# Kernel optimization log

Hardware: AMD Instinct MI355X
Metric: run time of the kernel (lower is better)

## Reference

```python
import jax, jax.numpy as jnp
import numpy as np

EPS = 1e-5

def layernorm(x, w, b):
    mu = jnp.mean(x, axis=-1, keepdims=True)
    xc = x - mu
    var = jnp.mean(xc * xc, axis=-1, keepdims=True)
    return xc * jax.lax.rsqrt(var + EPS) * w + b

def setup_inputs() -> dict:
    key = jax.random.key(0)
    ks = jax.random.split(key, 9)
    B, T, Nm, Nl = 8, 8, 1024, 64
    Vw, Tw, H, Dh = 1024, 2048, 8, 64
    inner = H * Dh  # 512
    s_q = 1.0 / np.sqrt(Tw)
    s_kv = 1.0 / np.sqrt(Vw)
    s_o = 1.0 / np.sqrt(inner)
    return {
        "x": jax.random.normal(ks[0], (B, T, Nm, Vw), jnp.float32),
        "latents": jax.random.normal(ks[1], (B, T, Nl, Tw), jnp.float32),
        "nm_w": jnp.ones((Vw,), jnp.float32),
        "nm_b": jnp.zeros((Vw,), jnp.float32),
        "nl_w": jnp.ones((Tw,), jnp.float32),
        "nl_b": jnp.zeros((Tw,), jnp.float32),
        "Wq": jax.random.normal(ks[2], (Tw, inner), jnp.float32) * s_q,
        "Wkv": jax.random.normal(ks[3], (Vw, 2 * inner), jnp.float32) * s_kv,
        "Wout": jax.random.normal(ks[4], (inner, Tw), jnp.float32) * s_o,
    }

def reference(x, latents, nm_w, nm_b, nl_w, nl_b, Wq, Wkv, Wout):
    H, Dh = 8, 64
    scale = Dh ** (-0.5)
    B, T, Nm, _ = x.shape
    Nl = latents.shape[2]
    xn = layernorm(x, nm_w, nm_b)          # (B,T,Nm,Vw)
    ln = layernorm(latents, nl_w, nl_b)    # (B,T,Nl,Tw)
    q = (ln @ Wq).reshape(B, T, Nl, H, Dh)           # b t i h d
    kv = xn @ Wkv                                     # (B,T,Nm,2*inner)
    k, v = jnp.split(kv, 2, axis=-1)
    k = k.reshape(B, T, Nm, H, Dh)                    # b t j h d
    v = v.reshape(B, T, Nm, H, Dh)
    sim = jnp.einsum('btihd,btjhd->bthij', q * scale, k)  # (B,T,H,Nl,Nm)
    attn = jax.nn.softmax(sim, axis=-1)
    out = jnp.einsum('bthij,btjhd->btihd', attn, v)       # (B,T,Nl,H,Dh)
    out = out.reshape(B, T, Nl, H * Dh)
    return out @ Wout                                     # (B,T,Nl,Tw)
```

## Files before the change

kernel.cpp:

```cpp
#include <hip/hip_runtime.h>

typedef __attribute__((ext_vector_type(8))) short bfrag8;
typedef __attribute__((ext_vector_type(4))) float f32x4;

typedef const unsigned int __attribute__((address_space(1)))* gas1_u32;
typedef unsigned int __attribute__((address_space(3)))* gas3_u32;

#define DEV __device__ __forceinline__

DEV unsigned short f2bf(float f) {
  unsigned int u = __builtin_bit_cast(unsigned int, f);
  u += 0x7fffu + ((u >> 16) & 1u);
  return (unsigned short)(u >> 16);
}

DEV void gload_lds16(const void* g, void* l) {
  __builtin_amdgcn_global_load_lds((gas1_u32)g, (gas3_u32)l, 16, 0, 0);
}

__global__ __launch_bounds__(256) void k_pre(
    const float* __restrict__ x, unsigned short* __restrict__ xb,
    float* __restrict__ mu, float* __restrict__ rstd,
    const float* __restrict__ lat, const float* __restrict__ nl_w,
    const float* __restrict__ nl_b, unsigned short* __restrict__ lnb,
    const float* __restrict__ Wq,   unsigned short* __restrict__ WqT,
    const float* __restrict__ Wkv,  unsigned short* __restrict__ WkvT,
    const float* __restrict__ Wout, unsigned short* __restrict__ WoutT,
    const float* __restrict__ nm_w, const float* __restrict__ nm_b,
    float* __restrict__ part)
{
  __shared__ float smem[32 * 33];
  const int bid = blockIdx.x, tid = threadIdx.x;
  const int wid = tid >> 6, lane = tid & 63;

  if (bid < 16384) {
    const int row = bid * 4 + wid;
    const float* base = x + (size_t)row * 1024;
    float4 v[4];
    #pragma unroll
    for (int i = 0; i < 4; ++i) v[i] = ((const float4*)base)[i * 64 + lane];
    float s = 0.f, q = 0.f;
    #pragma unroll
    for (int i = 0; i < 4; ++i) {
      s += v[i].x + v[i].y + v[i].z + v[i].w;
      q += v[i].x*v[i].x + v[i].y*v[i].y + v[i].z*v[i].z + v[i].w*v[i].w;
    }
    #pragma unroll
    for (int off = 32; off >= 1; off >>= 1) { s += __shfl_xor(s, off); q += __shfl_xor(q, off); }
    const float m  = s * (1.0f/1024.0f);
    const float var = q * (1.0f/1024.0f) - m * m;
    const float rs = rsqrtf(var + 1e-5f);
    if (lane == 0) { mu[row] = m; rstd[row] = rs; }
    unsigned short* ob = xb + (size_t)row * 1024;
    #pragma unroll
    for (int i = 0; i < 4; ++i) {
      ushort4 o;
      o.x = f2bf(v[i].x); o.y = f2bf(v[i].y); o.z = f2bf(v[i].z); o.w = f2bf(v[i].w);
      ((ushort4*)ob)[i * 64 + lane] = o;
    }
    return;
  }
  if (bid < 20480) {
    const int row = bid - 16384;
    const float* base = lat + (size_t)row * 2048;
    const float4 v0 = ((const float4*)base)[tid];
    const float4 v1 = ((const float4*)base)[256 + tid];
    float s = v0.x+v0.y+v0.z+v0.w + v1.x+v1.y+v1.z+v1.w;
    float q = v0.x*v0.x+v0.y*v0.y+v0.z*v0.z+v0.w*v0.w
            + v1.x*v1.x+v1.y*v1.y+v1.z*v1.z+v1.w*v1.w;
    #pragma unroll
    for (int off = 32; off >= 1; off >>= 1) { s += __shfl_xor(s, off); q += __shfl_xor(q, off); }
    if (lane == 0) { smem[wid] = s; smem[4 + wid] = q; }
    __syncthreads();
    s = smem[0] + smem[1] + smem[2] + smem[3];
    q = smem[4] + smem[5] + smem[6] + smem[7];
    const float m  = s * (1.0f/2048.0f);
    const float var = q * (1.0f/2048.0f) - m * m;
    const float rs = rsqrtf(var + 1e-5f);
    const float4 w0 = ((const float4*)nl_w)[tid], w1 = ((const float4*)nl_w)[256 + tid];
    const float4 b0 = ((const float4*)nl_b)[tid], b1 = ((const float4*)nl_b)[256 + tid];
    ushort4 o0, o1;
    o0.x = f2bf((v0.x - m) * rs * w0.x + b0.x);
    o0.y = f2bf((v0.y - m) * rs * w0.y + b0.y);
    o0.z = f2bf((v0.z - m) * rs * w0.z + b0.z);
    o0.w = f2bf((v0.w - m) * rs * w0.w + b0.w);
    o1.x = f2bf((v1.x - m) * rs * w1.x + b1.x);
    o1.y = f2bf((v1.y - m) * rs * w1.y + b1.y);
    o1.z = f2bf((v1.z - m) * rs * w1.z + b1.z);
    o1.w = f2bf((v1.w - m) * rs * w1.w + b1.w);
    ((ushort4*)(lnb + (size_t)row * 2048))[tid] = o0;
    ((ushort4*)(lnb + (size_t)row * 2048))[256 + tid] = o1;
    return;
  }
  if (bid < 23552) {
    int tb = bid - 20480;
    const float* src; unsigned short* dst; int Kd, N; const float* rsc; float sc;
    if (tb < 1024)      { src = Wq;   dst = WqT;   Kd = 2048; N = 512;  rsc = nullptr; sc = 0.125f; }
    else if (tb < 2048) { tb -= 1024; src = Wkv;  dst = WkvT;  Kd = 1024; N = 1024; rsc = nm_w;   sc = 1.0f; }
    else                { tb -= 2048; src = Wout; dst = WoutT; Kd = 512;  N = 2048; rsc = nullptr; sc = 1.0f; }
    float (*tile)[33] = (float(*)[33])smem;
    const int tx = tid & 31, ty = tid >> 5;
    const int ntiles = N >> 5;
    const int k0 = (tb / ntiles) << 5;
    const int n0 = (tb % ntiles) << 5;
    #pragma unroll
    for (int r = 0; r < 4; ++r) {
      const int kk = ty + r * 8;
      float v = src[(size_t)(k0 + kk) * N + n0 + tx] * sc;
      if (rsc) v *= rsc[k0 + kk];
      tile[kk][tx] = v;
    }
    __syncthreads();
    #pragma unroll
    for (int r = 0; r < 4; ++r) {
      const int nn = ty + r * 8;
      dst[(size_t)(n0 + nn) * Kd + k0 + tx] = f2bf(tile[tx][nn]);
    }
    return;
  }
  {
    const int cb = bid - 23552;
    const int kc = cb >> 2;
    const int n  = (cb & 3) * 256 + tid;
    float s1 = 0.f, s2 = 0.f;
    const int k0 = kc * 64;
    for (int k = k0; k < k0 + 64; ++k) {
      const float wv = Wkv[(size_t)k * 1024 + n];
      s1 += nm_w[k] * wv;
      s2 += nm_b[k] * wv;
    }
    part[(size_t)(kc * 2 + 0) * 1024 + n] = s1;
    part[(size_t)(kc * 2 + 1) * 1024 + n] = s2;
  }
}

__global__ __launch_bounds__(256) void k_c1c2_red(
    const float* __restrict__ part, float* __restrict__ c1, float* __restrict__ c2)
{
  const int n = blockIdx.x * 256 + threadIdx.x;
  float s1 = 0.f, s2 = 0.f;
  #pragma unroll
  for (int kc = 0; kc < 16; ++kc) {
    s1 += part[(size_t)(kc * 2 + 0) * 1024 + n];
    s2 += part[(size_t)(kc * 2 + 1) * 1024 + n];
  }
  c1[n] = s1; c2[n] = s2;
}

#define BAR8   __builtin_amdgcn_s_barrier()
#define GATE4  asm volatile("s_waitcnt vmcnt(4)\n\ts_barrier" ::: "memory")

__global__ __launch_bounds__(512, 2) void k_mm(
    const unsigned short* __restrict__ A,
    const unsigned short* __restrict__ Bt,
    unsigned short* __restrict__ C,
    const float* __restrict__ mu, const float* __restrict__ rstd,
    const float* __restrict__ c1, const float* __restrict__ c2,
    const unsigned short* __restrict__ Aq,
    const unsigned short* __restrict__ Bq,
    unsigned short* __restrict__ Cq)
{
  __shared__ __attribute__((aligned(16))) char lds[131072];
  const int tid = threadIdx.x;
  const int wid = tid >> 6, lane = tid & 63;
  const int g = lane >> 4, c = lane & 15;

  if (blockIdx.x < 1024) {
    constexpr int NKT = 16;
    int bid = blockIdx.x;
    bid = (bid & 7) * 128 + (bid >> 3);
    const int mt = bid >> 2, nt = bid & 3;
    const int wr = wid >> 2, wc = wid & 3;
    const int MO = wr * 128, NO = wc * 64;

    const unsigned short* gA = A + (size_t)mt * 256 * 1024;
    const unsigned short* gB = Bt + (size_t)nt * 256 * 1024;

    const f32x4 zz = {0.f, 0.f, 0.f, 0.f};
    f32x4 acc[8][4];
    #pragma unroll
    for (int m = 0; m < 8; ++m)
      #pragma unroll
      for (int n = 0; n < 4; ++n) acc[m][n] = zz;

    auto stageA = [&](int buf, int kk, int kt) {
      #pragma unroll
      for (int i = 0; i < 2; ++i) {
        const int o = (i * 512 + tid) * 16;
        const int row = o >> 6;
        const int ss = ((((o >> 4) & 3) - (row >> 1)) & 3);
        gload_lds16((const char*)(gA + (size_t)row * 1024 + kt * 64 + kk * 32) + ss * 16,
                    lds + buf * 32768 + kk * 16384 + o);
      }
    };
    auto stageB = [&](int buf, int kk, int kt) {
      #pragma unroll
      for (int i = 0; i < 2; ++i) {
        const int o = (i * 512 + tid) * 16;
        const int row = o >> 6;
        const int ss = ((((o >> 4) & 3) - (row >> 1)) & 3);
        gload_lds16((const char*)(gB + (size_t)row * 1024 + kt * 64 + kk * 32) + ss * 16,
                    lds + 65536 + buf * 32768 + kk * 16384 + o);
      }
    };
    auto rdA = [&](int buf, int kk, int m) -> bfrag8 {
      const int row = MO + m * 16 + c;
      return *(const bfrag8*)(lds + buf * 32768 + kk * 16384 + row * 64
                              + (((g + (row >> 1)) & 3) << 4));
    };
    auto rdB = [&](int buf, int kk, int n) -> bfrag8 {
      const int row = NO + n * 16 + c;
      return *(const bfrag8*)(lds + 65536 + buf * 32768 + kk * 16384 + row * 64
                              + (((g + (row >> 1)) & 3) << 4));
    };

    bfrag8 a[8], b0[4], b1[4];

    auto tile4 = [&](int buf, int sb, int ukt) {
      #pragma unroll
      for (int m = 0; m < 8; ++m) a[m] = rdA(buf, 0, m);
      #pragma unroll
      for (int n = 0; n < 4; ++n) b0[n] = rdB(buf, 0, n);
      stageA(sb, 0, ukt);
      __builtin_amdgcn_s_setprio(1);
      #pragma unroll
      for (int m = 0; m < 8; ++m) {
        acc[m][0] = __builtin_amdgcn_mfma_f32_16x16x32_bf16(a[m], b0[0], acc[m][0], 0, 0, 0);
        acc[m][1] = __builtin_amdgcn_mfma_f32_16x16x32_bf16(a[m], b0[1], acc[m][1], 0, 0, 0);
      }
      __builtin_amdgcn_s_setprio(0);
      GATE4;
      #pragma unroll
      for (int n = 0; n < 4; ++n) b1[n] = rdB(buf, 1, n);
      stageB(sb, 0, ukt);
      __builtin_amdgcn_s_setprio(1);
      #pragma unroll
      for (int m = 0; m < 8; ++m) {
        acc[m][2] = __builtin_amdgcn_mfma_f32_16x16x32_bf16(a[m], b0[2], acc[m][2], 0, 0, 0);
        acc[m][3] = __builtin_amdgcn_mfma_f32_16x16x32_bf16(a[m], b0[3], acc[m][3], 0, 0, 0);
      }
      __builtin_amdgcn_s_setprio(0);
      GATE4;
      #pragma unroll
      for (int m = 0; m < 8; ++m) a[m] = rdA(buf, 1, m);
      stageB(sb, 1, ukt);
      __builtin_amdgcn_s_setprio(1);
      #pragma unroll
      for (int m = 0; m < 8; ++m) {
        acc[m][0] = __builtin_amdgcn_mfma_f32_16x16x32_bf16(a[m], b1[0], acc[m][0], 0, 0, 0);
        acc[m][1] = __builtin_amdgcn_mfma_f32_16x16x32_bf16(a[m], b1[1], acc[m][1], 0, 0, 0);
      }
      __builtin_amdgcn_s_setprio(0);
      BAR8;
      stageA(sb, 1, ukt);
      __builtin_amdgcn_s_setprio(1);
      #pragma unroll
      for (int m = 0; m < 8; ++m) {
        acc[m][2] = __builtin_amdgcn_mfma_f32_16x16x32_bf16(a[m], b1[2], acc[m][2], 0, 0, 0);
        acc[m][3] = __builtin_amdgcn_mfma_f32_16x16x32_bf16(a[m], b1[3], acc[m][3], 0, 0, 0);
      }
      __builtin_amdgcn_s_setprio(0);
      GATE4;
    };

    stageA(0, 0, 0); stageB(0, 0, 0); stageB(0, 1, 0); stageA(0, 1, 0);
    GATE4;

    for (int t = 0; t < NKT; t += 2) {
      const int u2 = (t + 2 < NKT) ? t + 2 : 0;
      tile4(0, 1, t + 1);
      tile4(1, 0, u2);
    }
    asm volatile("s_waitcnt vmcnt(0)" ::: "memory");

    #pragma unroll
    for (int m = 0; m < 8; ++m) {
      #pragma unroll
      for (int j = 0; j < 4; ++j) {
        const size_t orow = (size_t)mt * 256 + MO + m * 16 + g * 4 + j;
        const float rs = rstd[orow], muv = mu[orow];
        #pragma unroll
        for (int n = 0; n < 4; ++n) {
          const int gcol = nt * 256 + NO + n * 16 + c;
          const float v = rs * (acc[m][n][j] - muv * c1[gcol]) + c2[gcol];
          C[orow * 1024 + gcol] = f2bf(v);
        }
      }
    }
    return;
  }

  {
    constexpr int BK = 64, MF = 4, NF = 2;
    int lb = blockIdx.x - 1024;
    lb = (lb & 7) * 16 + (lb >> 3);
    const int mt = lb >> 1, nt = lb & 1;
    const int NO = (wid & 7) * 32;
    const int MO = 0;

    const unsigned short* gA = Aq + (size_t)mt * 64 * 2048;
    const unsigned short* gB = Bq + (size_t)nt * 256 * 2048;
    auto asb = [&](int buf) { return lds + buf * 8192; };
    auto bsb = [&](int buf) { return lds + 16384 + buf * 32768; };

    const f32x4 zz = {0.f, 0.f, 0.f, 0.f};
    f32x4 acc[MF][NF];
    #pragma unroll
    for (int m = 0; m < MF; ++m)
      #pragma unroll
      for (int n = 0; n < NF; ++n) acc[m][n] = zz;

    auto stage = [&](int buf, int kt) {
      {
        const int o = tid * 16;
        const int row = o >> 7;
        const int sg = (((o >> 4) & 7) - row) & 7;
        gload_lds16((const char*)(gA + (size_t)row * 2048 + kt * BK) + sg * 16,
                    asb(buf) + o);
      }
      #pragma unroll
      for (int i = 0; i < 4; ++i) {
        const int o = (i * 512 + tid) * 16;
        const int row = o >> 7;
        const int sg = (((o >> 4) & 7) - row) & 7;
        gload_lds16((const char*)(gB + (size_t)row * 2048 + kt * BK) + sg * 16,
                    bsb(buf) + o);
      }
    };
    auto compute = [&](int buf) {
      #pragma unroll
      for (int kk = 0; kk < 2; ++kk) {
        bfrag8 af[MF], bf[NF];
        #pragma unroll
        for (int m = 0; m < MF; ++m) {
          const int rw = MO + m * 16 + c;
          af[m] = *(const bfrag8*)((const char*)asb(buf) + rw * 128
                                   + (((kk * 4 + g + rw) & 7) << 4));
        }
        #pragma unroll
        for (int n = 0; n < NF; ++n) {
          const int rw = NO + n * 16 + c;
          bf[n] = *(const bfrag8*)((const char*)bsb(buf) + rw * 128
                                   + (((kk * 4 + g + rw) & 7) << 4));
        }
        #pragma unroll
        for (int m = 0; m < MF; ++m)
          #pragma unroll
          for (int n = 0; n < NF; ++n)
            acc[m][n] = __builtin_amdgcn_mfma_f32_16x16x32_bf16(af[m], bf[n], acc[m][n], 0, 0, 0);
      }
    };

    const int nkt = 2048 / BK;
    stage(0, 0);
    __syncthreads();
    for (int t = 0; t < nkt; t += 2) {
      if (t + 1 < nkt) stage(1, t + 1);
      compute(0);
      __syncthreads();
      if (t + 2 < nkt) stage(0, t + 2);
      if (t + 1 < nkt) compute(1);
      __syncthreads();
    }

    #pragma unroll
    for (int m = 0; m < MF; ++m) {
      #pragma unroll
      for (int j = 0; j < 4; ++j) {
        const size_t orow = (size_t)mt * 64 + MO + m * 16 + g * 4 + j;
        #pragma unroll
        for (int n = 0; n < NF; ++n) {
          const int gcol = nt * 256 + NO + n * 16 + c;
          Cq[orow * 512 + gcol] = f2bf(acc[m][n][j]);
        }
      }
    }
  }
}

template<int BM, int BN, int WM, int WN, int NT, int MODE>
__global__ __launch_bounds__(NT, 2) void k_gemm(
    const unsigned short* __restrict__ A, int lda,
    const unsigned short* __restrict__ Bt, int ldb,
    int K, int mtiles, int ntiles,
    void* __restrict__ Cout, int ldc)
{
  constexpr int BK = 64;
  constexpr int NW = NT / 64;
  constexpr int MF = (BM / WM) / 16;
  constexpr int NF = (BN / WN) / 16;
  constexpr int LA = (BM * BK) / (8 * NT);
  constexpr int LB = (BN * BK) / (8 * NT);
  static_assert(WM * WN == NW, "wave grid");
  static_assert(LA >= 1 && LB >= 1, "tile too small for NT");

  __shared__ __attribute__((aligned(16))) unsigned short As[2][BM * BK];
  __shared__ __attribute__((aligned(16))) unsigned short Bs[2][BN * BK];

  int bid = blockIdx.x;
  {
    const int nwg = gridDim.x;
    if ((nwg & 7) == 0) {
      const int q = nwg >> 3;
      bid = (bid & 7) * q + (bid >> 3);
    }
  }
  const int mt = bid / ntiles, nt = bid % ntiles;
  const int tid = threadIdx.x;
  const int wid = tid >> 6, lane = tid & 63;
  const int g = lane >> 4, c = lane & 15;
  const int wr = wid / WN, wc = wid % WN;
  const int MO = wr * (BM / WM), NO = wc * (BN / WN);

  const unsigned short* gA = A + (size_t)mt * BM * lda;
  const unsigned short* gB = Bt + (size_t)nt * BN * ldb;

  const f32x4 zz = {0.f, 0.f, 0.f, 0.f};
  f32x4 acc[MF][NF];
  #pragma unroll
  for (int m = 0; m < MF; ++m)
    #pragma unroll
    for (int n = 0; n < NF; ++n) acc[m][n] = zz;

  auto stage = [&](int buf, int kt) {
    #pragma unroll
    for (int i = 0; i < LA; ++i) {
      const int o = (i * NT + tid) * 16;
      const int row = o >> 7;
      const int sg = (((o >> 4) & 7) - row) & 7;
      gload_lds16((const char*)(gA + (size_t)row * lda + kt * BK) + sg * 16,
                  (char*)&As[buf][0] + o);
    }
    #pragma unroll
    for (int i = 0; i < LB; ++i) {
      const int o = (i * NT + tid) * 16;
      const int row = o >> 7;
      const int sg = (((o >> 4) & 7) - row) & 7;
      gload_lds16((const char*)(gB + (size_t)row * ldb + kt * BK) + sg * 16,
                  (char*)&Bs[buf][0] + o);
    }
  };

  auto compute = [&](int buf) {
    #pragma unroll
    for (int kk = 0; kk < 2; ++kk) {
      bfrag8 af[MF], bf[NF];
      #pragma unroll
      for (int m = 0; m < MF; ++m) {
        const int rw = MO + m * 16 + c;
        af[m] = *(const bfrag8*)((const char*)&As[buf][0] + rw * 128
                                 + (((kk * 4 + g + rw) & 7) << 4));
      }
      #pragma unroll
      for (int n = 0; n < NF; ++n) {
        const int rw = NO + n * 16 + c;
        bf[n] = *(const bfrag8*)((const char*)&Bs[buf][0] + rw * 128
                                 + (((kk * 4 + g + rw) & 7) << 4));
      }
      #pragma unroll
      for (int m = 0; m < MF; ++m)
        #pragma unroll
        for (int n = 0; n < NF; ++n)
          acc[m][n] = __builtin_amdgcn_mfma_f32_16x16x32_bf16(af[m], bf[n], acc[m][n], 0, 0, 0);
    }
  };

  const int nkt = K / BK;
  stage(0, 0);
  __syncthreads();
  for (int t = 0; t < nkt; t += 2) {
    if (t + 1 < nkt) stage(1, t + 1);
    compute(0);
    __syncthreads();
    if (t + 2 < nkt) stage(0, t + 2);
    if (t + 1 < nkt) compute(1);
    __syncthreads();
  }

  #pragma unroll
  for (int m = 0; m < MF; ++m) {
    #pragma unroll
    for (int j = 0; j < 4; ++j) {
      const size_t orow = (size_t)mt * BM + MO + m * 16 + g * 4 + j;
      #pragma unroll
      for (int n = 0; n < NF; ++n) {
        const int gcol = nt * BN + NO + n * 16 + c;
        const float v = acc[m][n][j];
        if constexpr (MODE == 2) ((float*)Cout)[orow * ldc + gcol] = v;
        else ((unsigned short*)Cout)[orow * ldc + gcol] = f2bf(v);
      }
    }
  }
}

__global__ __launch_bounds__(256) void k_attn(
    const unsigned short* __restrict__ q,
    const unsigned short* __restrict__ kv,
    unsigned short* __restrict__ ao)
{
  __shared__ __attribute__((aligned(16))) unsigned short Vt[64 * 64];
  const int bid = blockIdx.x;
  const int bt = bid >> 3, h = bid & 7;
  const int tid = threadIdx.x;
  const int wid = tid >> 6, lane = tid & 63;
  const int g = lane >> 4, c = lane & 15;

  const size_t qoff = ((size_t)bt * 64 + wid * 16 + c) * 512 + h * 64;
  const bfrag8 qf0 = *(const bfrag8*)(q + qoff + g * 8);
  const bfrag8 qf1 = *(const bfrag8*)(q + qoff + 32 + g * 8);

  const f32x4 zz = {0.f, 0.f, 0.f, 0.f};
  f32x4 o[4] = {zz, zz, zz, zz};
  float m_run = -1e30f, l_run = 0.f;

  const size_t kvbase = (size_t)bt * 1024 * 1024;
  const unsigned short* kbase = kv + kvbase + h * 64;
  const unsigned short* vbase = kv + kvbase + 512 + h * 64;

  for (int ch = 0; ch < 16; ++ch) {
    #pragma unroll
    for (int rr = 0; rr < 2; ++rr) {
      const int key = rr * 32 + (tid >> 3);
      const int d0 = (tid & 7) * 8;
      const bfrag8 vv = *(const bfrag8*)(vbase + (size_t)(ch * 64 + key) * 1024 + d0);
      #pragma unroll
      for (int j = 0; j < 8; ++j)
        Vt[(d0 + j) * 64 + (key ^ (j << 3))] = (unsigned short)vv[j];
    }
    __syncthreads();
    #pragma unroll
    for (int ks = 0; ks < 2; ++ks) {
      const int kb = ch * 64 + ks * 32;
      f32x4 s[2];
      #pragma unroll
      for (int t = 0; t < 2; ++t) {
        const int kr = ((c >> 2) << 3) + (t << 2) + (c & 3);
        const unsigned short* krow = kbase + (size_t)(kb + kr) * 1024;
        s[t] = zz;
        s[t] = __builtin_amdgcn_mfma_f32_16x16x32_bf16(*(const bfrag8*)(krow + g * 8),      qf0, s[t], 0, 0, 0);
        s[t] = __builtin_amdgcn_mfma_f32_16x16x32_bf16(*(const bfrag8*)(krow + 32 + g * 8), qf1, s[t], 0, 0, 0);
      }
      float pm = s[0][0];
      #pragma unroll
      for (int i = 1; i < 4; ++i) pm = fmaxf(pm, s[0][i]);
      #pragma unroll
      for (int i = 0; i < 4; ++i) pm = fmaxf(pm, s[1][i]);
      pm = fmaxf(pm, __shfl_xor(pm, 16));
      pm = fmaxf(pm, __shfl_xor(pm, 32));
      const float mn = fmaxf(m_run, pm);
      const float alpha = __expf(m_run - mn);
      float p[8];
      #pragma unroll
      for (int i = 0; i < 4; ++i) p[i]     = __expf(s[0][i] - mn);
      #pragma unroll
      for (int i = 0; i < 4; ++i) p[4 + i] = __expf(s[1][i] - mn);
      float ts = 0.f;
      #pragma unroll
      for (int i = 0; i < 8; ++i) ts += p[i];
      ts += __shfl_xor(ts, 16);
      ts += __shfl_xor(ts, 32);
      l_run = l_run * alpha + ts;
      m_run = mn;
      float ar[4];
      #pragma unroll
      for (int rj = 0; rj < 4; ++rj) ar[rj] = __shfl(alpha, g * 4 + rj);
      #pragma unroll
      for (int db = 0; db < 4; ++db)
        #pragma unroll
        for (int j = 0; j < 4; ++j) o[db][j] *= ar[j];
      bfrag8 pa;
      #pragma unroll
      for (int i = 0; i < 8; ++i) pa[i] = (short)f2bf(p[i]);
      #pragma unroll
      for (int db = 0; db < 4; ++db) {
        const int d = db * 16 + c;
        const bfrag8 vb = *(const bfrag8*)(Vt + d * 64 + ((ks * 32 + g * 8) ^ ((c & 7) << 3)));
        o[db] = __builtin_amdgcn_mfma_f32_16x16x32_bf16(pa, vb, o[db], 0, 0, 0);
      }
    }
    __syncthreads();
  }
  float lr[4];
  #pragma unroll
  for (int rj = 0; rj < 4; ++rj) lr[rj] = __shfl(l_run, g * 4 + rj);
  #pragma unroll
  for (int db = 0; db < 4; ++db)
    #pragma unroll
    for (int j = 0; j < 4; ++j) {
      const float val = o[db][j] / lr[j];
      ao[((size_t)bt * 64 + wid * 16 + g * 4 + j) * 512 + h * 64 + db * 16 + c] = f2bf(val);
    }
}

extern "C" void kernel_launch(void* const* d_in, const int* in_sizes, int n_in,
                              void* d_out, int out_size, void* d_ws, size_t ws_size,
                              hipStream_t stream)
{
  const float* x    = (const float*)d_in[0];
  const float* lat  = (const float*)d_in[1];
  const float* nm_w = (const float*)d_in[2];
  const float* nm_b = (const float*)d_in[3];
  const float* nl_w = (const float*)d_in[4];
  const float* nl_b = (const float*)d_in[5];
  const float* Wq   = (const float*)d_in[6];
  const float* Wkv  = (const float*)d_in[7];
  const float* Wout = (const float*)d_in[8];

  char* p = (char*)d_ws;
  auto take = [&](size_t bytes) { char* r = p; p += (bytes + 255) & ~(size_t)255; return r; };
  unsigned short* xb    = (unsigned short*)take(64ull * 1024 * 1024 * 2);
  unsigned short* kvb   = (unsigned short*)take(64ull * 1024 * 1024 * 2);
  unsigned short* lnb   = (unsigned short*)take(4096ull * 2048 * 2);
  unsigned short* qbuf  = (unsigned short*)take(4096ull * 512 * 2);
  unsigned short* aob   = (unsigned short*)take(4096ull * 512 * 2);
  unsigned short* WqT   = (unsigned short*)take(512ull * 2048 * 2);
  unsigned short* WkvT  = (unsigned short*)take(1024ull * 1024 * 2);
  unsigned short* WoutT = (unsigned short*)take(2048ull * 512 * 2);
  float* muv  = (float*)take(65536ull * 4);
  float* rsd  = (float*)take(65536ull * 4);
  float* c1   = (float*)take(1024 * 4);
  float* c2   = (float*)take(1024 * 4);
  float* part = (float*)take(32ull * 1024 * 4);
  if ((size_t)(p - (char*)d_ws) > ws_size) return;

  k_pre<<<dim3(23616), 256, 0, stream>>>(x, xb, muv, rsd,
                                         lat, nl_w, nl_b, lnb,
                                         Wq, WqT, Wkv, WkvT, Wout, WoutT,
                                         nm_w, nm_b, part);
  k_c1c2_red<<<dim3(4), 256, 0, stream>>>(part, c1, c2);

  k_mm<<<dim3(1152), 512, 0, stream>>>(xb, WkvT, kvb, muv, rsd, c1, c2,
                                       lnb, WqT, qbuf);

  k_attn<<<dim3(512), 256, 0, stream>>>(qbuf, kvb, aob);

  k_gemm<64, 128, 1, 4, 256, 2><<<dim3(1024), 256, 0, stream>>>(
      aob, 512, WoutT, 512, 512, 64, 16, d_out, 2048);
}
```

Measured before the change: 356.0 us.

## Fuse x layernorm stats and bf16 conversion into KV GEMM A-loading

Removes the separate pass that read x, computed row mean/rstd and wrote a bf16 copy. The KV GEMM now loads fp32 x directly into registers, converts to bf16 while writing LDS, and accumulates row statistics on the fly for the epilogue. This saves a full 256MB read plus 128MB write round trip. In exchange, each of the four N-tiles re-reads fp32 x (twice the bytes of the bf16 copy), register pressure rises, occupancy drops to one block per CU, and the pipeline schedule changes.

```diff
diff --git a/kernel.cpp b/kernel.cpp
--- a/kernel.cpp
+++ b/kernel.cpp
@@ -19,8 +19,6 @@
 }
 
 __global__ __launch_bounds__(256) void k_pre(
-    const float* __restrict__ x, unsigned short* __restrict__ xb,
-    float* __restrict__ mu, float* __restrict__ rstd,
     const float* __restrict__ lat, const float* __restrict__ nl_w,
     const float* __restrict__ nl_b, unsigned short* __restrict__ lnb,
     const float* __restrict__ Wq,   unsigned short* __restrict__ WqT,
@@ -33,35 +31,8 @@
   const int bid = blockIdx.x, tid = threadIdx.x;
   const int wid = tid >> 6, lane = tid & 63;
 
-  if (bid < 16384) {
-    const int row = bid * 4 + wid;
-    const float* base = x + (size_t)row * 1024;
-    float4 v[4];
-    #pragma unroll
-    for (int i = 0; i < 4; ++i) v[i] = ((const float4*)base)[i * 64 + lane];
-    float s = 0.f, q = 0.f;
-    #pragma unroll
-    for (int i = 0; i < 4; ++i) {
-      s += v[i].x + v[i].y + v[i].z + v[i].w;
-      q += v[i].x*v[i].x + v[i].y*v[i].y + v[i].z*v[i].z + v[i].w*v[i].w;
-    }
-    #pragma unroll
-    for (int off = 32; off >= 1; off >>= 1) { s += __shfl_xor(s, off); q += __shfl_xor(q, off); }
-    const float m  = s * (1.0f/1024.0f);
-    const float var = q * (1.0f/1024.0f) - m * m;
-    const float rs = rsqrtf(var + 1e-5f);
-    if (lane == 0) { mu[row] = m; rstd[row] = rs; }
-    unsigned short* ob = xb + (size_t)row * 1024;
-    #pragma unroll
-    for (int i = 0; i < 4; ++i) {
-      ushort4 o;
-      o.x = f2bf(v[i].x); o.y = f2bf(v[i].y); o.z = f2bf(v[i].z); o.w = f2bf(v[i].w);
-      ((ushort4*)ob)[i * 64 + lane] = o;
-    }
-    return;
-  }
-  if (bid < 20480) {
-    const int row = bid - 16384;
+  if (bid < 4096) {
+    const int row = bid;
     const float* base = lat + (size_t)row * 2048;
     const float4 v0 = ((const float4*)base)[tid];
     const float4 v1 = ((const float4*)base)[256 + tid];
@@ -92,8 +63,8 @@
     ((ushort4*)(lnb + (size_t)row * 2048))[256 + tid] = o1;
     return;
   }
-  if (bid < 23552) {
-    int tb = bid - 20480;
+  if (bid < 7168) {
+    int tb = bid - 4096;
     const float* src; unsigned short* dst; int Kd, N; const float* rsc; float sc;
     if (tb < 1024)      { src = Wq;   dst = WqT;   Kd = 2048; N = 512;  rsc = nullptr; sc = 0.125f; }
     else if (tb < 2048) { tb -= 1024; src = Wkv;  dst = WkvT;  Kd = 1024; N = 1024; rsc = nm_w;   sc = 1.0f; }
@@ -119,7 +90,7 @@
     return;
   }
   {
-    const int cb = bid - 23552;
+    const int cb = bid - 7168;
     const int kc = cb >> 2;
     const int n  = (cb & 3) * 256 + tid;
     float s1 = 0.f, s2 = 0.f;
@@ -147,20 +118,17 @@
   c1[n] = s1; c2[n] = s2;
 }
 
-#define BAR8   __builtin_amdgcn_s_barrier()
-#define GATE4  asm volatile("s_waitcnt vmcnt(4)\n\ts_barrier" ::: "memory")
-
-__global__ __launch_bounds__(512, 2) void k_mm(
-    const unsigned short* __restrict__ A,
+__global__ __launch_bounds__(512, 1) void k_mm(
+    const float* __restrict__ X,
     const unsigned short* __restrict__ Bt,
     unsigned short* __restrict__ C,
-    const float* __restrict__ mu, const float* __restrict__ rstd,
     const float* __restrict__ c1, const float* __restrict__ c2,
     const unsigned short* __restrict__ Aq,
     const unsigned short* __restrict__ Bq,
     unsigned short* __restrict__ Cq)
 {
   __shared__ __attribute__((aligned(16))) char lds[131072];
+  __shared__ float sstat[256][2];
   const int tid = threadIdx.x;
   const int wid = tid >> 6, lane = tid & 63;
   const int g = lane >> 4, c = lane & 15;
@@ -173,8 +141,12 @@
     const int wr = wid >> 2, wc = wid & 3;
     const int MO = wr * 128, NO = wc * 64;
 
-    const unsigned short* gA = A + (size_t)mt * 256 * 1024;
     const unsigned short* gB = Bt + (size_t)nt * 256 * 1024;
+    const int arow = tid >> 1, asl = tid & 1;
+    const int rho = (arow >> 1) & 3;
+    const int ps0 = (2 * asl + 0 + rho) & 3;
+    const int ps1 = (2 * asl + 1 + rho) & 3;
+    const float* gX = X + (size_t)(mt * 256 + arow) * 1024 + asl * 16;
 
     const f32x4 zz = {0.f, 0.f, 0.f, 0.f};
     f32x4 acc[8][4];
@@ -183,15 +155,31 @@
       #pragma unroll
       for (int n = 0; n < 4; ++n) acc[m][n] = zz;
 
-    auto stageA = [&](int buf, int kk, int kt) {
-      #pragma unroll
-      for (int i = 0; i < 2; ++i) {
-        const int o = (i * 512 + tid) * 16;
-        const int row = o >> 6;
-        const int ss = ((((o >> 4) & 3) - (row >> 1)) & 3);
-        gload_lds16((const char*)(gA + (size_t)row * 1024 + kt * 64 + kk * 32) + ss * 16,
-                    lds + buf * 32768 + kk * 16384 + o);
-      }
+    float4 ax[2][4];
+    float ssum = 0.f, sq = 0.f;
+
+    auto loadA = [&](int kt) {
+      #pragma unroll
+      for (int kk = 0; kk < 2; ++kk)
+        #pragma unroll
+        for (int i = 0; i < 4; ++i)
+          ax[kk][i] = *(const float4*)(gX + (size_t)kt * 64 + kk * 32 + i * 4);
+    };
+    auto putA = [&](int buf, int kk, int accum) {
+      unsigned int w[8];
+      #pragma unroll
+      for (int i = 0; i < 4; ++i) {
+        const float4 v = ax[kk][i];
+        if (accum) {
+          ssum += v.x + v.y + v.z + v.w;
+          sq   += v.x*v.x + v.y*v.y + v.z*v.z + v.w*v.w;
+        }
+        w[2*i]   = (unsigned)f2bf(v.x) | ((unsigned)f2bf(v.y) << 16);
+        w[2*i+1] = (unsigned)f2bf(v.z) | ((unsigned)f2bf(v.w) << 16);
+      }
+      char* base = lds + buf * 32768 + kk * 16384 + arow * 64;
+      *(uint4*)(base + ps0 * 16) = make_uint4(w[0], w[1], w[2], w[3]);
+      *(uint4*)(base + ps1 * 16) = make_uint4(w[4], w[5], w[6], w[7]);
     };
     auto stageB = [&](int buf, int kk, int kt) {
       #pragma unroll
@@ -216,12 +204,13 @@
 
     bfrag8 a[8], b0[4], b1[4];
 
-    auto tile4 = [&](int buf, int sb, int ukt) {
+    auto tile4 = [&](int buf, int sb, int ukt, int accum) {
       #pragma unroll
       for (int m = 0; m < 8; ++m) a[m] = rdA(buf, 0, m);
       #pragma unroll
       for (int n = 0; n < 4; ++n) b0[n] = rdB(buf, 0, n);
-      stageA(sb, 0, ukt);
+      loadA(ukt);
+      stageB(sb, 0, ukt);
       __builtin_amdgcn_s_setprio(1);
       #pragma unroll
       for (int m = 0; m < 8; ++m) {
@@ -229,10 +218,11 @@
         acc[m][1] = __builtin_amdgcn_mfma_f32_16x16x32_bf16(a[m], b0[1], acc[m][1], 0, 0, 0);
       }
       __builtin_amdgcn_s_setprio(0);
-      GATE4;
+      asm volatile("s_waitcnt vmcnt(10)\n\ts_barrier" ::: "memory");
       #pragma unroll
       for (int n = 0; n < 4; ++n) b1[n] = rdB(buf, 1, n);
-      stageB(sb, 0, ukt);
+      putA(sb, 0, accum);
+      stageB(sb, 1, ukt);
       __builtin_amdgcn_s_setprio(1);
       #pragma unroll
       for (int m = 0; m < 8; ++m) {
@@ -240,10 +230,10 @@
         acc[m][3] = __builtin_amdgcn_mfma_f32_16x16x32_bf16(a[m], b0[3], acc[m][3], 0, 0, 0);
       }
       __builtin_amdgcn_s_setprio(0);
-      GATE4;
+      asm volatile("s_barrier" ::: "memory");
       #pragma unroll
       for (int m = 0; m < 8; ++m) a[m] = rdA(buf, 1, m);
-      stageB(sb, 1, ukt);
+      putA(sb, 1, accum);
       __builtin_amdgcn_s_setprio(1);
       #pragma unroll
       for (int m = 0; m < 8; ++m) {
@@ -251,8 +241,7 @@
         acc[m][1] = __builtin_amdgcn_mfma_f32_16x16x32_bf16(a[m], b1[1], acc[m][1], 0, 0, 0);
       }
       __builtin_amdgcn_s_setprio(0);
-      BAR8;
-      stageA(sb, 1, ukt);
+      asm volatile("s_barrier" ::: "memory");
       __builtin_amdgcn_s_setprio(1);
       #pragma unroll
       for (int m = 0; m < 8; ++m) {
@@ -260,25 +249,37 @@
         acc[m][3] = __builtin_amdgcn_mfma_f32_16x16x32_bf16(a[m], b1[3], acc[m][3], 0, 0, 0);
       }
       __builtin_amdgcn_s_setprio(0);
-      GATE4;
-    };
-
-    stageA(0, 0, 0); stageB(0, 0, 0); stageB(0, 1, 0); stageA(0, 1, 0);
-    GATE4;
-
-    for (int t = 0; t < NKT; t += 2) {
-      const int u2 = (t + 2 < NKT) ? t + 2 : 0;
-      tile4(0, 1, t + 1);
-      tile4(1, 0, u2);
-    }
-    asm volatile("s_waitcnt vmcnt(0)" ::: "memory");
+      asm volatile("s_waitcnt vmcnt(2) lgkmcnt(0)\n\ts_barrier" ::: "memory");
+    };
+
+    loadA(0);
+    putA(0, 0, 1); putA(0, 1, 1);
+    stageB(0, 0, 0); stageB(0, 1, 0);
+    asm volatile("s_waitcnt vmcnt(0) lgkmcnt(0)\n\ts_barrier" ::: "memory");
+
+    for (int t = 0; t < NKT; ++t) {
+      const int real = (t + 1 < NKT);
+      tile4(t & 1, (t & 1) ^ 1, real ? t + 1 : 0, real);
+    }
+    asm volatile("s_waitcnt vmcnt(0) lgkmcnt(0)" ::: "memory");
+
+    ssum += __shfl_xor(ssum, 1);
+    sq   += __shfl_xor(sq, 1);
+    if (asl == 0) {
+      const float m = ssum * (1.0f / 1024.0f);
+      const float var = sq * (1.0f / 1024.0f) - m * m;
+      sstat[arow][0] = m;
+      sstat[arow][1] = rsqrtf(var + 1e-5f);
+    }
+    __syncthreads();
 
     #pragma unroll
     for (int m = 0; m < 8; ++m) {
       #pragma unroll
       for (int j = 0; j < 4; ++j) {
-        const size_t orow = (size_t)mt * 256 + MO + m * 16 + g * 4 + j;
-        const float rs = rstd[orow], muv = mu[orow];
+        const int rl = MO + m * 16 + g * 4 + j;
+        const size_t orow = (size_t)mt * 256 + rl;
+        const float muv = sstat[rl][0], rs = sstat[rl][1];
         #pragma unroll
         for (int n = 0; n < 4; ++n) {
           const int gcol = nt * 256 + NO + n * 16 + c;
@@ -608,7 +609,6 @@
 
   char* p = (char*)d_ws;
   auto take = [&](size_t bytes) { char* r = p; p += (bytes + 255) & ~(size_t)255; return r; };
-  unsigned short* xb    = (unsigned short*)take(64ull * 1024 * 1024 * 2);
   unsigned short* kvb   = (unsigned short*)take(64ull * 1024 * 1024 * 2);
   unsigned short* lnb   = (unsigned short*)take(4096ull * 2048 * 2);
   unsigned short* qbuf  = (unsigned short*)take(4096ull * 512 * 2);
@@ -616,21 +616,17 @@
   unsigned short* WqT   = (unsigned short*)take(512ull * 2048 * 2);
   unsigned short* WkvT  = (unsigned short*)take(1024ull * 1024 * 2);
   unsigned short* WoutT = (unsigned short*)take(2048ull * 512 * 2);
-  float* muv  = (float*)take(65536ull * 4);
-  float* rsd  = (float*)take(65536ull * 4);
   float* c1   = (float*)take(1024 * 4);
   float* c2   = (float*)take(1024 * 4);
   float* part = (float*)take(32ull * 1024 * 4);
   if ((size_t)(p - (char*)d_ws) > ws_size) return;
 
-  k_pre<<<dim3(23616), 256, 0, stream>>>(x, xb, muv, rsd,
-                                         lat, nl_w, nl_b, lnb,
-                                         Wq, WqT, Wkv, WkvT, Wout, WoutT,
-                                         nm_w, nm_b, part);
+  k_pre<<<dim3(7232), 256, 0, stream>>>(lat, nl_w, nl_b, lnb,
+                                        Wq, WqT, Wkv, WkvT, Wout, WoutT,
+                                        nm_w, nm_b, part);
   k_c1c2_red<<<dim3(4), 256, 0, stream>>>(part, c1, c2);
 
-  k_mm<<<dim3(1152), 512, 0, stream>>>(xb, WkvT, kvb, muv, rsd, c1, c2,
-                                       lnb, WqT, qbuf);
+  k_mm<<<dim3(1152), 512, 0, stream>>>(x, WkvT, kvb, c1, c2, lnb, WqT, qbuf);
 
   k_attn<<<dim3(512), 256, 0, stream>>>(qbuf, kvb, aob);
 
```

After: 871.1 us (median of 2 runs). 2.45x slower.
